# Kernel tuning notes

Measured on AMD Instinct MI355X. Metric: run time of the kernel, lower is better.

Reference implementation:

```python
import jax, jax.numpy as jnp
import numpy as np

N_NODES = 50000
N_EDGES = 800000
N_GRAPHS = 256
IN_DIM = 128
HID = 64
HEADS = 4
N_CLASSES = 2
NEG_SLOPE = 0.2


def gat_conv(h, W, attn_l, attn_r, bias, src, dst, n_heads, out_dim):
    """DGL-style GATConv. h: [N, Fin] -> [N, H, D]."""
    n = h.shape[0]
    feat = (h @ W).reshape(n, n_heads, out_dim)            # [N,H,D]
    el = jnp.sum(feat * attn_l, axis=-1)                   # [N,H]
    er = jnp.sum(feat * attn_r, axis=-1)                   # [N,H]
    e = jax.nn.leaky_relu(el[src] + er[dst], NEG_SLOPE)    # [E,H]
    # edge softmax over incoming edges of each dst node (numerically stable)
    emax = jax.ops.segment_max(e, dst, num_segments=n)     # [N,H]
    emax = jnp.where(jnp.isfinite(emax), emax, 0.0)
    ee = jnp.exp(e - emax[dst])                            # [E,H]
    denom = jax.ops.segment_sum(ee, dst, num_segments=n)   # [N,H]
    alpha = ee / jnp.maximum(denom, 1e-9)[dst]             # [E,H]
    msg = alpha[:, :, None] * feat[src]                    # [E,H,D]
    rst = jax.ops.segment_sum(msg, dst, num_segments=n)    # [N,H,D]
    return rst + bias.reshape(1, n_heads, out_dim)


def setup_inputs() -> dict:
    key = jax.random.key(0)
    ks = jax.random.split(key, 16)
    h = jax.random.normal(ks[0], (N_NODES, IN_DIM), dtype=jnp.float32)
    src = jax.random.randint(ks[1], (N_EDGES,), 0, N_NODES, dtype=jnp.int32)
    dst = jax.random.randint(ks[2], (N_EDGES,), 0, N_NODES, dtype=jnp.int32)
    graph_ids = jnp.sort(jax.random.randint(ks[3], (N_NODES,), 0, N_GRAPHS, dtype=jnp.int32))
    s1 = 1.0 / np.sqrt(IN_DIM)
    s2 = 1.0 / np.sqrt(HID * HEADS)
    sc = 1.0 / np.sqrt(HID)
    W1 = jax.random.normal(ks[4], (IN_DIM, HEADS * HID), dtype=jnp.float32) * s1
    attn_l1 = jax.random.normal(ks[5], (HEADS, HID), dtype=jnp.float32) * sc
    attn_r1 = jax.random.normal(ks[6], (HEADS, HID), dtype=jnp.float32) * sc
    b1 = jnp.zeros((HEADS * HID,), dtype=jnp.float32)
    W2 = jax.random.normal(ks[7], (HEADS * HID, 1 * HID), dtype=jnp.float32) * s2
    attn_l2 = jax.random.normal(ks[8], (1, HID), dtype=jnp.float32) * sc
    attn_r2 = jax.random.normal(ks[9], (1, HID), dtype=jnp.float32) * sc
    b2 = jnp.zeros((HID,), dtype=jnp.float32)
    Wc = jax.random.normal(ks[10], (HID, N_CLASSES), dtype=jnp.float32) * sc
    bc = jnp.zeros((N_CLASSES,), dtype=jnp.float32)
    return {"h": h, "src": src, "dst": dst, "graph_ids": graph_ids,
            "W1": W1, "attn_l1": attn_l1, "attn_r1": attn_r1, "b1": b1,
            "W2": W2, "attn_l2": attn_l2, "attn_r2": attn_r2, "b2": b2,
            "Wc": Wc, "bc": bc}


def reference(h, src, dst, graph_ids, W1, attn_l1, attn_r1, b1,
              W2, attn_l2, attn_r2, b2, Wc, bc):
    # layer 1: [N, IN] -> [N, HEADS, HID] -> relu -> flatten heads
    x = jax.nn.relu(gat_conv(h, W1, attn_l1, attn_r1, b1, src, dst, HEADS, HID))
    x = x.reshape(N_NODES, HEADS * HID)
    # layer 2: single head -> [N, HID]
    x = jax.nn.relu(gat_conv(x, W2, attn_l2, attn_r2, b2, src, dst, 1, HID))
    x = x.reshape(N_NODES, HID)
    # dropout p=0.3 is identity at eval time
    # AvgPooling: mean of node features per graph
    sums = jax.ops.segment_sum(x, graph_ids, num_segments=N_GRAPHS)      # [G,HID]
    cnts = jax.ops.segment_sum(jnp.ones((N_NODES,), x.dtype), graph_ids,
                               num_segments=N_GRAPHS)                    # [G]
    pooled = sums / jnp.maximum(cnts, 1.0)[:, None]
    return pooled @ Wc + bc                                              # [G, n_classes]
```

## Files before the change

### kernel.cpp

```cpp
#include <hip/hip_runtime.h>
#include <math.h>

#define NN 50000
#define NE 800000
#define NG 256
#define IND 128

typedef __bf16 bf16_t;
typedef bf16_t bf16x8 __attribute__((ext_vector_type(8)));
typedef float f32x4 __attribute__((ext_vector_type(4)));
typedef float floatx2 __attribute__((ext_vector_type(2)));
typedef unsigned short ushortx8 __attribute__((ext_vector_type(8)));

__device__ __forceinline__ float lrelu(float x) { return fmaxf(x, 0.2f * x); }
__device__ __forceinline__ float b2f(unsigned short u) {
  return __uint_as_float(((unsigned)u) << 16);
}
__device__ __forceinline__ unsigned short f2b(float f) {
  unsigned u = __float_as_uint(f);
  return (unsigned short)((u + 0x7fffu + ((u >> 16) & 1u)) >> 16);
}
__device__ __forceinline__ float sel4(float v0, float v1, float v2, float v3, int g) {
  float a01 = (g & 1) ? v1 : v0;
  float a23 = (g & 1) ? v3 : v2;
  return (g & 2) ? a23 : a01;
}

__global__ __launch_bounds__(256) void k_prep(const float* __restrict__ W1,
                                              const int* __restrict__ dst,
                                              unsigned short* __restrict__ w1t_hi,
                                              int* __restrict__ counts) {
  int tid = blockIdx.x * 256 + threadIdx.x;
  if (tid < 256 * IND) {
    int c = tid >> 7, k = tid & 127;
    w1t_hi[tid] = f2b(W1[(size_t)k * 256 + c]);
  }
  if (tid < NE) atomicAdd(&counts[dst[tid]], 1);
}

__global__ __launch_bounds__(256) void k_gemm1(const float* __restrict__ h,
                                               const unsigned short* __restrict__ w1t_hi,
                                               const float* __restrict__ al,
                                               const float* __restrict__ ar,
                                               unsigned int* __restrict__ feat1f8,
                                               float4* __restrict__ el1,
                                               float4* __restrict__ er1) {
  __shared__ unsigned short w1s[256 * IND];
  int t = threadIdx.x;
  for (int i = t; i < 4096; i += 256) {
    int c = i >> 4, k8 = i & 15;
    ushortx8 v = ((const ushortx8*)w1t_hi)[i];
    int byte = (c * 256 + k8 * 16) ^ ((c & 7) << 4);
    *(ushortx8*)((char*)w1s + byte) = v;
  }
  __syncthreads();
  int w = t >> 6, l = t & 63;
  int c0 = l & 15, kg = l >> 4;
  int rw = blockIdx.x * 64 + w * 16;
  int arow = rw + c0;
  if (arow >= NN) arow = NN - 1;
  const float4* hp = (const float4*)h + (size_t)arow * 32 + kg * 2;
  f32x4 acc[16] = {};
#pragma unroll
  for (int ks = 0; ks < 4; ks++) {
    float4 v0 = hp[ks * 8], v1 = hp[ks * 8 + 1];
    float f[8] = {v0.x, v0.y, v0.z, v0.w, v1.x, v1.y, v1.z, v1.w};
    ushortx8 uh, ul;
#pragma unroll
    for (int j = 0; j < 8; j++) {
      unsigned short hj = f2b(f[j]);
      uh[j] = hj;
      ul[j] = f2b(f[j] - b2f(hj));
    }
    bf16x8 ah = *(bf16x8*)&uh;
    bf16x8 alo = *(bf16x8*)&ul;
#pragma unroll
    for (int n = 0; n < 16; n++) {
      int col = n * 16 + c0;
      int byte = (col * 256 + (ks * 4 + kg) * 16) ^ ((col & 7) << 4);
      bf16x8 b = *(const bf16x8*)(const void*)((const char*)w1s + byte);
      acc[n] = __builtin_amdgcn_mfma_f32_16x16x32_bf16(alo, b, acc[n], 0, 0, 0);
      acc[n] = __builtin_amdgcn_mfma_f32_16x16x32_bf16(ah, b, acc[n], 0, 0, 0);
    }
  }
  float alv[16], arv[16];
#pragma unroll
  for (int n = 0; n < 16; n++) {
    int ai = (n >> 2) * 64 + (n & 3) * 16 + c0;
    alv[n] = al[ai];
    arv[n] = ar[ai];
  }
#pragma unroll
  for (int j = 0; j < 4; j++) {
    int node = rw + kg * 4 + j;
    bool ok = node < NN;
    float pl[4] = {0.f, 0.f, 0.f, 0.f}, pr[4] = {0.f, 0.f, 0.f, 0.f};
#pragma unroll
    for (int dq = 0; dq < 4; dq++) {
      float v0 = acc[dq][j], v1 = acc[4 | dq][j], v2 = acc[8 | dq][j], v3 = acc[12 | dq][j];
      if (ok) {
        int u = __builtin_amdgcn_cvt_pk_fp8_f32(v0, v1, 0, false);
        u = __builtin_amdgcn_cvt_pk_fp8_f32(v2, v3, u, true);
        feat1f8[(size_t)node * 64 + dq * 16 + c0] = (unsigned)u;
      }
    }
#pragma unroll
    for (int n = 0; n < 16; n++) {
      float cv = acc[n][j];
      int hh = n >> 2;
      pl[hh] += cv * alv[n];
      pr[hh] += cv * arv[n];
    }
#pragma unroll
    for (int off = 1; off < 16; off <<= 1) {
#pragma unroll
      for (int hh = 0; hh < 4; hh++) {
        pl[hh] += __shfl_xor(pl[hh], off);
        pr[hh] += __shfl_xor(pr[hh], off);
      }
    }
    if (c0 == 0 && ok) {
      el1[node] = make_float4(pl[0], pl[1], pl[2], pl[3]);
      er1[node] = make_float4(pr[0], pr[1], pr[2], pr[3]);
    }
  }
}

#define NSB ((NN + 1023) / 1024)
__global__ __launch_bounds__(1024) void k_scanA(const int* __restrict__ counts,
                                                int* __restrict__ bsums) {
  int gid = blockIdx.x * 1024 + threadIdx.x;
  int v = (gid < NN) ? counts[gid] : 0;
#pragma unroll
  for (int off = 32; off; off >>= 1) v += __shfl_xor(v, off);
  __shared__ int ws[16];
  int w = threadIdx.x >> 6, l = threadIdx.x & 63;
  if (l == 0) ws[w] = v;
  __syncthreads();
  if (threadIdx.x == 0) {
    int s = 0;
#pragma unroll
    for (int i = 0; i < 16; i++) s += ws[i];
    bsums[blockIdx.x] = s;
  }
}

__global__ __launch_bounds__(64) void k_scanB(const int* __restrict__ bsums,
                                              int* __restrict__ boffs) {
  int l = threadIdx.x;
  int orig = (l < NSB) ? bsums[l] : 0;
  int v = orig;
#pragma unroll
  for (int off = 1; off < 64; off <<= 1) {
    int tv = __shfl_up(v, off);
    if (l >= off) v += tv;
  }
  if (l < NSB) boffs[l] = v - orig;
}

__global__ __launch_bounds__(1024) void k_scanC(const int* __restrict__ counts,
                                                const int* __restrict__ boffs,
                                                int* __restrict__ offs) {
  int gid = blockIdx.x * 1024 + threadIdx.x;
  int orig = (gid < NN) ? counts[gid] : 0;
  int v = orig;
  int w = threadIdx.x >> 6, l = threadIdx.x & 63;
#pragma unroll
  for (int off = 1; off < 64; off <<= 1) {
    int tv = __shfl_up(v, off);
    if (l >= off) v += tv;
  }
  __shared__ int ws[16];
  if (l == 63) ws[w] = v;
  __syncthreads();
  int woff = 0;
#pragma unroll
  for (int i = 0; i < 16; i++)
    if (i < w) woff += ws[i];
  if (gid < NN) offs[gid] = boffs[blockIdx.x] + woff + v - orig;
  if (gid == 0) offs[NN] = NE;
}

__global__ void k_scatter(const int* __restrict__ src, const int* __restrict__ dst,
                          const int* __restrict__ offs, int* __restrict__ cursor,
                          int2* __restrict__ sd) {
  int e = blockIdx.x * blockDim.x + threadIdx.x;
  if (e >= NE) return;
  int d = dst[e];
  int p = atomicAdd(&cursor[d], 1);
  int2 v;
  v.x = src[e];
  v.y = d;
  sd[offs[d] + p] = v;
}

__global__ __launch_bounds__(256) void k_edge1(const int2* __restrict__ sd,
                                               const float4* __restrict__ el1,
                                               const float4* __restrict__ er1,
                                               float4* __restrict__ ee1) {
  int i = blockIdx.x * 256 + threadIdx.x;
  if (i >= NE) return;
  int2 p = sd[i];
  float4 l = el1[p.x], r = er1[p.y];
  float4 o;
  o.x = __expf(lrelu(l.x + r.x));
  o.y = __expf(lrelu(l.y + r.y));
  o.z = __expf(lrelu(l.z + r.z));
  o.w = __expf(lrelu(l.w + r.w));
  ee1[i] = o;
}

__global__ __launch_bounds__(256) void k_agg1(const int* __restrict__ offs, const int2* __restrict__ sd,
                                              const float4* __restrict__ ee1,
                                              const unsigned int* __restrict__ feat1f8,
                                              const float* __restrict__ b1,
                                              unsigned short* __restrict__ x1b) {
  int wid = (blockIdx.x * 256 + threadIdx.x) >> 6;
  int lane = threadIdx.x & 63;
  if (wid >= NN) return;
  int g = lane >> 4, q = lane & 15;
  int start = offs[wid], end = offs[wid + 1];
  float a[4][4] = {};
  float ds0 = 0.f, ds1 = 0.f, ds2 = 0.f, ds3 = 0.f;
  for (int i = start; i < end; i += 4) {
    int e = i + g;
    bool valid = e < end;
    int ec = valid ? e : end - 1;
    int s = sd[ec].x;
    float4 wv = ee1[ec];
    if (!valid) { wv.x = 0.f; wv.y = 0.f; wv.z = 0.f; wv.w = 0.f; }
    uint4 u = *(const uint4*)(feat1f8 + (size_t)s * 64 + q * 4);
#pragma unroll
    for (int dj = 0; dj < 4; dj++) {
      unsigned uu = (&u.x)[dj];
      floatx2 lo = __builtin_amdgcn_cvt_pk_f32_fp8(uu, false);
      floatx2 hi = __builtin_amdgcn_cvt_pk_f32_fp8(uu, true);
      a[dj][0] += wv.x * lo[0];
      a[dj][1] += wv.y * lo[1];
      a[dj][2] += wv.z * hi[0];
      a[dj][3] += wv.w * hi[1];
    }
    ds0 += wv.x; ds1 += wv.y; ds2 += wv.z; ds3 += wv.w;
  }
#pragma unroll
  for (int off = 16; off < 64; off <<= 1) {
#pragma unroll
    for (int dj = 0; dj < 4; dj++) {
#pragma unroll
      for (int hh = 0; hh < 4; hh++) a[dj][hh] += __shfl_xor(a[dj][hh], off);
    }
    ds0 += __shfl_xor(ds0, off);
    ds1 += __shfl_xor(ds1, off);
    ds2 += __shfl_xor(ds2, off);
    ds3 += __shfl_xor(ds3, off);
  }
  float dsg = sel4(ds0, ds1, ds2, ds3, g);
  float inv = 1.f / fmaxf(dsg, 1e-9f);
  float4 bb = *(const float4*)(b1 + g * 64 + q * 4);
  ushort4 ov;
  ov.x = f2b(fmaxf(sel4(a[0][0], a[0][1], a[0][2], a[0][3], g) * inv + bb.x, 0.f));
  ov.y = f2b(fmaxf(sel4(a[1][0], a[1][1], a[1][2], a[1][3], g) * inv + bb.y, 0.f));
  ov.z = f2b(fmaxf(sel4(a[2][0], a[2][1], a[2][2], a[2][3], g) * inv + bb.z, 0.f));
  ov.w = f2b(fmaxf(sel4(a[3][0], a[3][1], a[3][2], a[3][3], g) * inv + bb.w, 0.f));
  *(ushort4*)(x1b + (size_t)wid * 256 + g * 64 + q * 4) = ov;
}

__global__ __launch_bounds__(256) void k_gemm2(const unsigned short* __restrict__ x1b,
                                               const float* __restrict__ W2,
                                               const float* __restrict__ al2,
                                               const float* __restrict__ ar2,
                                               unsigned int* __restrict__ feat2f8,
                                               float* __restrict__ el2,
                                               float* __restrict__ er2) {
  __shared__ unsigned short w2t[64 * 256];
  int t = threadIdx.x;
  for (int i = t; i < 64 * 256; i += 256) {
    int k = i >> 6, col = i & 63;
    int kg = k >> 3;
    int s = (col * 32 + kg) ^ (col & 7);
    w2t[s * 8 + (k & 7)] = f2b(W2[i]);
  }
  __syncthreads();
  int w = t >> 6, l = t & 63;
  int rw = blockIdx.x * 64 + w * 16;
  int arow = rw + (l & 15);
  if (arow >= NN) arow = NN - 1;
  const unsigned short* aptr = x1b + (size_t)arow * 256 + (l >> 4) * 8;
  f32x4 acc[4] = {};
#pragma unroll
  for (int ks = 0; ks < 8; ks++) {
    bf16x8 a = *(const bf16x8*)(const void*)(aptr + ks * 32);
#pragma unroll
    for (int n = 0; n < 4; n++) {
      int colg = n * 16 + (l & 15);
      int kg = ks * 4 + (l >> 4);
      int s = (colg * 32 + kg) ^ (colg & 7);
      bf16x8 b = *(const bf16x8*)(const void*)&w2t[s * 8];
      acc[n] = __builtin_amdgcn_mfma_f32_16x16x32_bf16(a, b, acc[n], 0, 0, 0);
    }
  }
  float al2v[4], ar2v[4];
#pragma unroll
  for (int n = 0; n < 4; n++) { al2v[n] = al2[n * 16 + (l & 15)]; ar2v[n] = ar2[n * 16 + (l & 15)]; }
#pragma unroll
  for (int j = 0; j < 4; j++) {
    int node = rw + (l >> 4) * 4 + j;
    float pl = 0.f, pr = 0.f;
    float c0v = acc[0][j], c1v = acc[1][j], c2v = acc[2][j], c3v = acc[3][j];
    if (node < NN) {
      int u = __builtin_amdgcn_cvt_pk_fp8_f32(c0v, c1v, 0, false);
      u = __builtin_amdgcn_cvt_pk_fp8_f32(c2v, c3v, u, true);
      feat2f8[(size_t)node * 16 + (l & 15)] = (unsigned)u;
    }
    pl = c0v * al2v[0] + c1v * al2v[1] + c2v * al2v[2] + c3v * al2v[3];
    pr = c0v * ar2v[0] + c1v * ar2v[1] + c2v * ar2v[2] + c3v * ar2v[3];
#pragma unroll
    for (int off = 1; off < 16; off <<= 1) {
      pl += __shfl_xor(pl, off);
      pr += __shfl_xor(pr, off);
    }
    if ((l & 15) == 0 && node < NN) { el2[node] = pl; er2[node] = pr; }
  }
}

__global__ __launch_bounds__(256) void k_edge2(const int2* __restrict__ sd,
                                               const float* __restrict__ el2,
                                               const float* __restrict__ er2,
                                               float* __restrict__ ee2) {
  int i = blockIdx.x * 256 + threadIdx.x;
  if (i >= NE) return;
  int2 p = sd[i];
  ee2[i] = __expf(lrelu(el2[p.x] + er2[p.y]));
}

__global__ __launch_bounds__(256) void k_agg2(const int* __restrict__ offs, const int2* __restrict__ sd,
                                              const float* __restrict__ ee2,
                                              const unsigned int* __restrict__ feat2f8,
                                              const float* __restrict__ b2, const int* __restrict__ gid,
                                              float* __restrict__ psum) {
  int wid = (blockIdx.x * 256 + threadIdx.x) >> 6;
  int lane = threadIdx.x & 63;
  if (wid >= NN) return;
  int g = lane >> 4, q = lane & 15;
  int start = offs[wid], end = offs[wid + 1];
  float a0 = 0.f, a1 = 0.f, a2 = 0.f, a3 = 0.f, dsum = 0.f;
  for (int i = start; i < end; i += 4) {
    int e = i + g;
    bool valid = e < end;
    int ec = valid ? e : end - 1;
    int s = sd[ec].x;
    float wv = valid ? ee2[ec] : 0.f;
    unsigned u = feat2f8[(size_t)s * 16 + q];
    floatx2 lo = __builtin_amdgcn_cvt_pk_f32_fp8(u, false);
    floatx2 hi = __builtin_amdgcn_cvt_pk_f32_fp8(u, true);
    a0 += wv * lo[0];
    a1 += wv * lo[1];
    a2 += wv * hi[0];
    a3 += wv * hi[1];
    dsum += wv;
  }
#pragma unroll
  for (int off = 16; off < 64; off <<= 1) {
    a0 += __shfl_xor(a0, off);
    a1 += __shfl_xor(a1, off);
    a2 += __shfl_xor(a2, off);
    a3 += __shfl_xor(a3, off);
    dsum += __shfl_xor(dsum, off);
  }
  float inv = 1.f / fmaxf(dsum, 1e-9f);
  float av = sel4(a0, a1, a2, a3, g);
  float v = fmaxf(av * inv + b2[lane], 0.f);
  atomicAdd(&psum[gid[wid] * 64 + lane], v);
}

__global__ __launch_bounds__(256) void k_head(const float* __restrict__ psum, const int* __restrict__ gid,
                                              const float* __restrict__ Wc, const float* __restrict__ bc,
                                              float* __restrict__ out) {
  int wid = (blockIdx.x * 256 + threadIdx.x) >> 6;
  int lane = threadIdx.x & 63;
  if (wid >= NG) return;
  int g = wid;
  int lo = 0, hi = NN;
  while (lo < hi) { int mid = (lo + hi) >> 1; if (gid[mid] < g) lo = mid + 1; else hi = mid; }
  int lb = lo;
  hi = NN;
  while (lo < hi) { int mid = (lo + hi) >> 1; if (gid[mid] < g + 1) lo = mid + 1; else hi = mid; }
  int cnt = lo - lb;
  float inv = 1.f / fmaxf((float)cnt, 1.f);
  float p = psum[g * 64 + lane] * inv;
  float a0 = p * Wc[lane * 2 + 0];
  float a1 = p * Wc[lane * 2 + 1];
#pragma unroll
  for (int off = 32; off; off >>= 1) { a0 += __shfl_xor(a0, off); a1 += __shfl_xor(a1, off); }
  if (lane == 0) { out[g * 2 + 0] = a0 + bc[0]; out[g * 2 + 1] = a1 + bc[1]; }
}

extern "C" void kernel_launch(void* const* d_in, const int* in_sizes, int n_in,
                              void* d_out, int out_size, void* d_ws, size_t ws_size,
                              hipStream_t stream) {
  const float* h = (const float*)d_in[0];
  const int* src = (const int*)d_in[1];
  const int* dst = (const int*)d_in[2];
  const int* gid = (const int*)d_in[3];
  const float* W1 = (const float*)d_in[4];
  const float* al1 = (const float*)d_in[5];
  const float* ar1 = (const float*)d_in[6];
  const float* b1 = (const float*)d_in[7];
  const float* W2 = (const float*)d_in[8];
  const float* al2 = (const float*)d_in[9];
  const float* ar2 = (const float*)d_in[10];
  const float* b2 = (const float*)d_in[11];
  const float* Wc = (const float*)d_in[12];
  const float* bc = (const float*)d_in[13];
  float* out = (float*)d_out;

  char* wsp = (char*)d_ws;
  size_t off = 0;
  auto take = [&](size_t bytes) -> void* {
    void* p = wsp + off;
    off = (off + bytes + 255) & ~(size_t)255;
    return p;
  };
  unsigned int* feat1f8 = (unsigned int*)take((size_t)NN * 256);
  unsigned short* x1b = (unsigned short*)take((size_t)NN * 256 * 2);
  unsigned int* feat2f8 = (unsigned int*)take((size_t)NN * 64);
  unsigned short* w1t_hi = (unsigned short*)take((size_t)256 * IND * 2);
  float4* el1 = (float4*)take((size_t)NN * 16);
  float4* er1 = (float4*)take((size_t)NN * 16);
  float* el2 = (float*)take((size_t)NN * 4);
  float* er2 = (float*)take((size_t)NN * 4);
  int* counts = (int*)take((size_t)NN * 4);
  int* offs = (int*)take((size_t)(NN + 1) * 4);
  int* cursor = (int*)take((size_t)NN * 4);
  int2* sd = (int2*)take((size_t)NE * 8);
  float4* ee1 = (float4*)take((size_t)NE * 16);
  float* ee2 = (float*)take((size_t)NE * 4);
  float* psum = (float*)take((size_t)NG * 64 * 4);
  int* bsums = (int*)take((size_t)NSB * 4);
  int* boffs = (int*)take((size_t)NSB * 4);

  hipMemsetAsync(counts, 0, (size_t)NN * 4, stream);
  hipMemsetAsync(cursor, 0, (size_t)NN * 4, stream);
  hipMemsetAsync(psum, 0, (size_t)NG * 64 * 4, stream);

  k_prep<<<(NE + 255) / 256, 256, 0, stream>>>(W1, dst, w1t_hi, counts);

  k_scanA<<<NSB, 1024, 0, stream>>>(counts, bsums);
  k_scanB<<<1, 64, 0, stream>>>(bsums, boffs);
  k_scanC<<<NSB, 1024, 0, stream>>>(counts, boffs, offs);
  k_scatter<<<(NE + 255) / 256, 256, 0, stream>>>(src, dst, offs, cursor, sd);

  k_gemm1<<<(NN + 63) / 64, 256, 0, stream>>>(h, w1t_hi, al1, ar1, feat1f8, el1, er1);
  k_edge1<<<(NE + 255) / 256, 256, 0, stream>>>(sd, el1, er1, ee1);
  k_agg1<<<(NN * 64 + 255) / 256, 256, 0, stream>>>(offs, sd, ee1, feat1f8, b1, x1b);

  k_gemm2<<<(NN + 63) / 64, 256, 0, stream>>>(x1b, W2, al2, ar2, feat2f8, el2, er2);
  k_edge2<<<(NE + 255) / 256, 256, 0, stream>>>(sd, el2, er2, ee2);
  k_agg2<<<(NN * 64 + 255) / 256, 256, 0, stream>>>(offs, sd, ee2, feat2f8, b2, gid, psum);

  k_head<<<(NG * 64 + 255) / 256, 256, 0, stream>>>(psum, gid, Wc, bc, out);
}
```

Before: 242.0 us.

## Replace global-atomic CSR scatter with two-pass bucketed partition; store edge weights bf16

The single-pass CSR scatter did one global atomic per edge and wrote to random locations. It is replaced by two kernels. The first partitions edges into 98 buckets of 512 destination nodes using shared-memory atomics and one global atomic per bucket per block. The second places each bucket's edges with shared-memory cursors. Separately, layer-1 edge exp weights are stored as bf16 instead of fp32, halving that buffer's traffic at some precision cost. The change adds an extra pass over an 8-byte-per-edge staging buffer, and the second kernel runs only 98 blocks, which may underuse the GPU.

```diff
diff --git a/kernel.cpp b/kernel.cpp
--- a/kernel.cpp
+++ b/kernel.cpp
@@ -5,6 +5,9 @@
 #define NE 800000
 #define NG 256
 #define IND 128
+#define NBUCK 98
+#define CHUNK 4096
+#define NPBLK ((NE + CHUNK - 1) / CHUNK)
 
 typedef __bf16 bf16_t;
 typedef bf16_t bf16x8 __attribute__((ext_vector_type(8)));
@@ -146,7 +149,8 @@
 }
 
 __global__ __launch_bounds__(64) void k_scanB(const int* __restrict__ bsums,
-                                              int* __restrict__ boffs) {
+                                              int* __restrict__ boffs,
+                                              int* __restrict__ bcursor) {
   int l = threadIdx.x;
   int orig = (l < NSB) ? bsums[l] : 0;
   int v = orig;
@@ -156,6 +160,7 @@
     if (l >= off) v += tv;
   }
   if (l < NSB) boffs[l] = v - orig;
+  for (int i = l; i < NBUCK; i += 64) bcursor[i] = 0;
 }
 
 __global__ __launch_bounds__(1024) void k_scanC(const int* __restrict__ counts,
@@ -181,37 +186,80 @@
   if (gid == 0) offs[NN] = NE;
 }
 
-__global__ void k_scatter(const int* __restrict__ src, const int* __restrict__ dst,
-                          const int* __restrict__ offs, int* __restrict__ cursor,
-                          int2* __restrict__ sd) {
-  int e = blockIdx.x * blockDim.x + threadIdx.x;
-  if (e >= NE) return;
-  int d = dst[e];
-  int p = atomicAdd(&cursor[d], 1);
-  int2 v;
-  v.x = src[e];
-  v.y = d;
-  sd[offs[d] + p] = v;
+__global__ __launch_bounds__(256) void k_part(const int* __restrict__ src, const int* __restrict__ dst,
+                                              const int* __restrict__ offs, int* __restrict__ bcursor,
+                                              int2* __restrict__ ebuf) {
+  __shared__ int lcnt[NBUCK];
+  __shared__ int lbase[NBUCK];
+  __shared__ int gb[NBUCK];
+  int t = threadIdx.x;
+  for (int i = t; i < NBUCK; i += 256) lcnt[i] = 0;
+  __syncthreads();
+  int e0 = blockIdx.x * CHUNK;
+  int sv[16], dv[16], rk[16];
+#pragma unroll
+  for (int i = 0; i < 16; i++) {
+    int e = e0 + i * 256 + t;
+    if (e < NE) {
+      sv[i] = src[e];
+      dv[i] = dst[e];
+      rk[i] = atomicAdd(&lcnt[dv[i] >> 9], 1);
+    }
+  }
+  __syncthreads();
+  for (int i = t; i < NBUCK; i += 256) {
+    lbase[i] = atomicAdd(&bcursor[i], lcnt[i]);
+    gb[i] = offs[i << 9];
+  }
+  __syncthreads();
+#pragma unroll
+  for (int i = 0; i < 16; i++) {
+    int e = e0 + i * 256 + t;
+    if (e < NE) {
+      int b = dv[i] >> 9;
+      int2 v;
+      v.x = sv[i];
+      v.y = dv[i];
+      ebuf[gb[b] + lbase[b] + rk[i]] = v;
+    }
+  }
+}
+
+__global__ __launch_bounds__(256) void k_scat2(const int2* __restrict__ ebuf, const int* __restrict__ offs,
+                                               int2* __restrict__ sd) {
+  __shared__ int lcur[512];
+  int b = blockIdx.x, t = threadIdx.x;
+  for (int i = t; i < 512; i += 256) lcur[i] = 0;
+  int n0 = b << 9;
+  int n1 = n0 + 512;
+  if (n1 > NN) n1 = NN;
+  int lo = offs[n0], hi = offs[n1];
+  __syncthreads();
+  for (int i = lo + t; i < hi; i += 256) {
+    int2 p = ebuf[i];
+    int pos = atomicAdd(&lcur[p.y - n0], 1);
+    sd[offs[p.y] + pos] = p;
+  }
 }
 
 __global__ __launch_bounds__(256) void k_edge1(const int2* __restrict__ sd,
                                                const float4* __restrict__ el1,
                                                const float4* __restrict__ er1,
-                                               float4* __restrict__ ee1) {
+                                               ushort4* __restrict__ ee1) {
   int i = blockIdx.x * 256 + threadIdx.x;
   if (i >= NE) return;
   int2 p = sd[i];
   float4 l = el1[p.x], r = er1[p.y];
-  float4 o;
-  o.x = __expf(lrelu(l.x + r.x));
-  o.y = __expf(lrelu(l.y + r.y));
-  o.z = __expf(lrelu(l.z + r.z));
-  o.w = __expf(lrelu(l.w + r.w));
+  ushort4 o;
+  o.x = f2b(__expf(lrelu(l.x + r.x)));
+  o.y = f2b(__expf(lrelu(l.y + r.y)));
+  o.z = f2b(__expf(lrelu(l.z + r.z)));
+  o.w = f2b(__expf(lrelu(l.w + r.w)));
   ee1[i] = o;
 }
 
 __global__ __launch_bounds__(256) void k_agg1(const int* __restrict__ offs, const int2* __restrict__ sd,
-                                              const float4* __restrict__ ee1,
+                                              const ushort4* __restrict__ ee1,
                                               const unsigned int* __restrict__ feat1f8,
                                               const float* __restrict__ b1,
                                               unsigned short* __restrict__ x1b) {
@@ -227,7 +275,9 @@
     bool valid = e < end;
     int ec = valid ? e : end - 1;
     int s = sd[ec].x;
-    float4 wv = ee1[ec];
+    ushort4 wq = ee1[ec];
+    float4 wv;
+    wv.x = b2f(wq.x); wv.y = b2f(wq.y); wv.z = b2f(wq.z); wv.w = b2f(wq.w);
     if (!valid) { wv.x = 0.f; wv.y = 0.f; wv.z = 0.f; wv.w = 0.f; }
     uint4 u = *(const uint4*)(feat1f8 + (size_t)s * 64 + q * 4);
 #pragma unroll
@@ -431,24 +481,25 @@
   float* er2 = (float*)take((size_t)NN * 4);
   int* counts = (int*)take((size_t)NN * 4);
   int* offs = (int*)take((size_t)(NN + 1) * 4);
-  int* cursor = (int*)take((size_t)NN * 4);
   int2* sd = (int2*)take((size_t)NE * 8);
-  float4* ee1 = (float4*)take((size_t)NE * 16);
+  int2* ebuf = (int2*)take((size_t)NE * 8);
+  ushort4* ee1 = (ushort4*)take((size_t)NE * 8);
   float* ee2 = (float*)take((size_t)NE * 4);
   float* psum = (float*)take((size_t)NG * 64 * 4);
   int* bsums = (int*)take((size_t)NSB * 4);
   int* boffs = (int*)take((size_t)NSB * 4);
+  int* bcursor = (int*)take((size_t)NBUCK * 4);
 
   hipMemsetAsync(counts, 0, (size_t)NN * 4, stream);
-  hipMemsetAsync(cursor, 0, (size_t)NN * 4, stream);
   hipMemsetAsync(psum, 0, (size_t)NG * 64 * 4, stream);
 
   k_prep<<<(NE + 255) / 256, 256, 0, stream>>>(W1, dst, w1t_hi, counts);
 
   k_scanA<<<NSB, 1024, 0, stream>>>(counts, bsums);
-  k_scanB<<<1, 64, 0, stream>>>(bsums, boffs);
+  k_scanB<<<1, 64, 0, stream>>>(bsums, boffs, bcursor);
   k_scanC<<<NSB, 1024, 0, stream>>>(counts, boffs, offs);
-  k_scatter<<<(NE + 255) / 256, 256, 0, stream>>>(src, dst, offs, cursor, sd);
+  k_part<<<NPBLK, 256, 0, stream>>>(src, dst, offs, bcursor, ebuf);
+  k_scat2<<<NBUCK, 256, 0, stream>>>(ebuf, offs, sd);
 
   k_gemm1<<<(NN + 63) / 64, 256, 0, stream>>>(h, w1t_hi, al1, ar1, feat1f8, el1, er1);
   k_edge1<<<(NE + 255) / 256, 256, 0, stream>>>(sd, el1, er1, ee1);
```

Result: faster. 226.8 us (-6.3%).
